# Kernel tuning notes

Hardware: AMD Instinct MI355X
Metric: run time of the kernel (lower is better)

The kernel has to match this reference:

```python
import jax, jax.numpy as jnp
import numpy as np

PATCH = 256
N = 50000
HC = 256  # height // PATCH
WC = 256  # width // PATCH

def _gauss_kernel():
    # GaussianSmoothing(channels=1, kernel_size=3, sigma=0.5)
    g = np.exp(-(((np.arange(3, dtype=np.float64) - 1.0) / 0.5) ** 2) / 2.0) / (0.5 * np.sqrt(2 * np.pi))
    k = np.outer(g, g)
    k = k / k.sum()
    return jnp.asarray(k, jnp.float32).reshape(1, 1, 3, 3)

def setup_inputs() -> dict:
    key = jax.random.key(0)
    ks = jax.random.split(key, 12)
    h = jax.random.normal(ks[0], (N, 1024), jnp.float32)
    # unique grid cells per patch (row-major), scaled back to pixel coords
    idx = jnp.arange(N, dtype=jnp.int64 if jax.config.jax_enable_x64 else jnp.int32)
    gx = idx % WC
    gy = idx // WC
    coords = jnp.stack([gx * PATCH, gy * PATCH], axis=1)
    eps = jax.random.normal(ks[1], (1, 1, HC, WC), jnp.float32)
    s = 0.02
    W1 = jax.random.normal(ks[2], (512, 1024), jnp.float32) * s
    b1 = jnp.zeros((512,), jnp.float32)
    W2a = jax.random.normal(ks[3], (256, 512), jnp.float32) * s
    b2a = jnp.zeros((256,), jnp.float32)
    W2b = jax.random.normal(ks[4], (256, 512), jnp.float32) * s
    b2b = jnp.zeros((256,), jnp.float32)
    W3 = jax.random.normal(ks[5], (2, 256), jnp.float32) * s
    b3 = jnp.zeros((2,), jnp.float32)
    Wc = jax.random.normal(ks[6], (2, 512), jnp.float32) * s
    bc = jnp.zeros((2,), jnp.float32)
    kernel = _gauss_kernel()
    return {"h": h, "coords": coords, "eps": eps,
            "W1": W1, "b1": b1, "W2a": W2a, "b2a": b2a, "W2b": W2b, "b2b": b2b,
            "W3": W3, "b3": b3, "Wc": Wc, "bc": bc, "kernel": kernel,
            "height": 65536, "width": 65536, "slide_label": 1}

def reference(h, coords, eps, W1, b1, W2a, b2a, W2b, b2b, W3, b3, Wc, bc, kernel, height, width, slide_label):
    hc, wc = height // PATCH, width // PATCH
    x = jax.nn.relu(h @ W1.T + b1)                      # [N,512] (dropout = eval identity)
    fa = jax.nn.sigmoid(x @ W2a.T + b2a)                # [N,256]
    fb = jnp.tanh(x @ W2b.T + b2b)                      # [N,256]
    params = (fa * fb) @ W3.T + b3                      # [N,2] -> (mu, logvar) per patch
    gx = coords[:, 0] // PATCH
    gy = coords[:, 1] // PATCH
    mu = jnp.zeros((1, hc, wc), x.dtype).at[0, gy, gx].set(params[:, 0])
    logvar = jnp.zeros((1, hc, wc), x.dtype).at[0, gy, gx].set(params[:, 1])
    prior_mu = jnp.array([-5.0, 0.0], x.dtype)[slide_label]
    prior_lv = jnp.array([-1.0, 3.0], x.dtype)[slide_label]
    kl_div = (prior_lv - logvar) / 2.0 + (logvar ** 2 + (prior_mu - mu) ** 2) / (2.0 * prior_lv ** 2) - 0.5
    mu_pad = jnp.pad(mu, ((0, 0), (1, 1), (1, 1)))[None]          # [1,1,hc+2,wc+2]
    mu_sm = jax.lax.conv_general_dilated(mu_pad, kernel, (1, 1), 'VALID')  # [1,1,hc,wc]
    samples = mu_sm + eps * jnp.exp(0.5 * logvar)                  # reparameterize, broadcast to [1,1,hc,wc]
    A = jax.nn.sigmoid(samples[0])                                 # [1,hc,wc]
    patch_A = A[0, gy, gx][None]                                   # gather -> [1,N]
    M = (patch_A @ x) / patch_A.sum()                              # [1,512]
    logits = M @ Wc.T + bc                                         # [1,n_classes]
    y_probs = jax.nn.softmax(logits, axis=1)
    top_idx = jax.lax.top_k(y_probs[:, 1], 1)[1]                   # top_k=1
    top_instance = logits[top_idx]                                 # [1,n_classes]
    Y_hat = jnp.argmax(top_instance, axis=1, keepdims=True)
    Y_prob = jax.nn.softmax(top_instance, axis=1)
    return (top_instance, Y_prob, Y_hat, kl_div, y_probs, patch_A)
```

## Files before the change

### kernel.cpp

```cpp
#include <hip/hip_runtime.h>
#include <hip/hip_bf16.h>
#include <cstdint>
#include <cstddef>

#define NPATCH 50000
#define GC 256

typedef __bf16 bf16x8 __attribute__((ext_vector_type(8)));
typedef float  f32x4  __attribute__((ext_vector_type(4)));
typedef float  f32x8  __attribute__((ext_vector_type(8)));

static constexpr size_t XB_OFF    = 0;
static constexpr size_t XB_BYTES  = (size_t)50048 * 512 * 2;
static constexpr size_t W1B_OFF   = XB_OFF + XB_BYTES;
static constexpr size_t W1B_BYTES = (size_t)512 * 1024 * 2;
static constexpr size_t W2AB_OFF  = W1B_OFF + W1B_BYTES;
static constexpr size_t W2X_BYTES = (size_t)256 * 512 * 2;
static constexpr size_t W2BB_OFF  = W2AB_OFF + W2X_BYTES;
static constexpr size_t MUG_OFF   = W2BB_OFF + W2X_BYTES;
static constexpr size_t LVG_OFF   = MUG_OFF + (size_t)65536 * 4;
static constexpr size_t AG_OFF    = LVG_OFF + (size_t)65536 * 4;
static constexpr size_t MPART_OFF = AG_OFF + (size_t)65536 * 4;
static constexpr size_t SUMA_OFF  = MPART_OFF + (size_t)512 * 4;
static constexpr size_t ZERO_BYTES = SUMA_OFF + 4 - MUG_OFF;

__device__ __forceinline__ unsigned short f2bf(float f) {
  union { float f; uint32_t u; } v; v.f = f;
  uint32_t u = v.u;
  uint32_t r = (u + 0x7FFFu + ((u >> 16) & 1u)) >> 16;
  return (unsigned short)r;
}
__device__ __forceinline__ float bf2f(uint32_t bits16) {
  union { uint32_t u; float f; } v; v.u = bits16 << 16; return v.f;
}
__device__ __forceinline__ unsigned short cvt_bf16(float f) {
  __bf16 b = (__bf16)f;
  return __builtin_bit_cast(unsigned short, b);
}
__device__ __forceinline__ void gld16(const void* g, void* l) {
  __builtin_amdgcn_global_load_lds(
      (const __attribute__((address_space(1))) void*)g,
      (__attribute__((address_space(3))) void*)l, 16, 0, 0);
}
__device__ __forceinline__ bf16x8 cvt8(const float4& f0, const float4& f1) {
  f32x8 fv;
  fv[0]=f0.x; fv[1]=f0.y; fv[2]=f0.z; fv[3]=f0.w;
  fv[4]=f1.x; fv[5]=f1.y; fv[6]=f1.z; fv[7]=f1.w;
  return __builtin_convertvector(fv, bf16x8);
}

__global__ void convert_weights(const float* __restrict__ W1,
                                const float* __restrict__ W2a,
                                const float* __restrict__ W2b,
                                unsigned short* __restrict__ W1b,
                                unsigned short* __restrict__ W2ab,
                                unsigned short* __restrict__ W2bb) {
  int i = blockIdx.x * 256 + threadIdx.x;
  if (i < 512 * 1024) W1b[i] = f2bf(W1[i]);
  if (i < 256 * 512) { W2ab[i] = f2bf(W2a[i]); W2bb[i] = f2bf(W2b[i]); }
}

__global__ __launch_bounds__(256) void gemm1(
    const float* __restrict__ h, const unsigned short* __restrict__ W1b,
    const float* __restrict__ b1, unsigned short* __restrict__ xb) {
  __shared__ __align__(16) unsigned short As[2][128 * 32];
  __shared__ __align__(16) unsigned short Bs[2][128 * 32];

  const int t  = threadIdx.x;
  const int l  = t & 63;
  const int w  = t >> 6;
  const int wr = w >> 1;
  const int wc = w & 1;
  const int g  = l >> 4;
  const int lr = l & 15;

  const int i = blockIdx.x;
  const int x = i & 7;
  const int s = i >> 3;
  const int n = s & 3;
  const int q = s >> 2;
  const int m = x + 8 * q;
  if (m >= 391) return;
  const int rowBase = m * 128;
  const int colBase = n * 128;

  const int ar = t >> 2;
  const int aj = t & 3;
  int gr0 = rowBase + ar;       if (gr0 >= NPATCH) gr0 = NPATCH - 1;
  int gr1 = rowBase + 64 + ar;  if (gr1 >= NPATCH) gr1 = NPATCH - 1;
  const float* asrc0 = h + (size_t)gr0 * 1024 + aj * 8;
  const float* asrc1 = h + (size_t)gr1 * 1024 + aj * 8;
  const unsigned short* bsrc0 = W1b + (size_t)(colBase + ar) * 1024 + aj * 8;
  const unsigned short* bsrc1 = bsrc0 + (size_t)64 * 1024;
  const int dst0 = t * 8;
  const int dst1 = 2048 + t * 8;

  f32x4 acc[4][4];
#pragma unroll
  for (int mm = 0; mm < 4; ++mm)
#pragma unroll
    for (int nn = 0; nn < 4; ++nn) acc[mm][nn] = (f32x4){0.f, 0.f, 0.f, 0.f};

  float4 s00, s01, s10, s11;
  {
    float4 t00 = *(const float4*)(asrc0 + 0);
    float4 t01 = *(const float4*)(asrc0 + 4);
    float4 t10 = *(const float4*)(asrc1 + 0);
    float4 t11 = *(const float4*)(asrc1 + 4);
    gld16(bsrc0, &Bs[0][dst0]);
    gld16(bsrc1, &Bs[0][dst1]);
    *(bf16x8*)&As[0][dst0] = cvt8(t00, t01);
    *(bf16x8*)&As[0][dst1] = cvt8(t10, t11);
    s00 = *(const float4*)(asrc0 + 32);
    s01 = *(const float4*)(asrc0 + 36);
    s10 = *(const float4*)(asrc1 + 32);
    s11 = *(const float4*)(asrc1 + 36);
  }
  __syncthreads();

  int cur = 0;
  for (int kt = 0; kt < 32; ++kt) {
    if (kt < 31) {
      gld16(bsrc0 + (kt + 1) * 32, &Bs[cur ^ 1][dst0]);
      gld16(bsrc1 + (kt + 1) * 32, &Bs[cur ^ 1][dst1]);
      *(bf16x8*)&As[cur ^ 1][dst0] = cvt8(s00, s01);
      *(bf16x8*)&As[cur ^ 1][dst1] = cvt8(s10, s11);
      if (kt < 30) {
        s00 = *(const float4*)(asrc0 + (kt + 2) * 32);
        s01 = *(const float4*)(asrc0 + (kt + 2) * 32 + 4);
        s10 = *(const float4*)(asrc1 + (kt + 2) * 32);
        s11 = *(const float4*)(asrc1 + (kt + 2) * 32 + 4);
      }
    }
    bf16x8 af[4], bfr[4];
#pragma unroll
    for (int mm = 0; mm < 4; ++mm)
      af[mm] = *(const bf16x8*)&As[cur][(wr * 64 + mm * 16 + lr) * 32 + g * 8];
#pragma unroll
    for (int nn = 0; nn < 4; ++nn)
      bfr[nn] = *(const bf16x8*)&Bs[cur][(wc * 64 + nn * 16 + lr) * 32 + g * 8];
#pragma unroll
    for (int mm = 0; mm < 4; ++mm)
#pragma unroll
      for (int nn = 0; nn < 4; ++nn)
        acc[mm][nn] = __builtin_amdgcn_mfma_f32_16x16x32_bf16(af[mm], bfr[nn], acc[mm][nn], 0, 0, 0);
    __syncthreads();
    cur ^= 1;
  }

  float b1v[4];
#pragma unroll
  for (int nn = 0; nn < 4; ++nn) b1v[nn] = b1[colBase + wc * 64 + nn * 16 + lr];
#pragma unroll
  for (int mm = 0; mm < 4; ++mm) {
    const int rb0 = rowBase + wr * 64 + mm * 16 + g * 4;
#pragma unroll
    for (int r = 0; r < 4; ++r) {
      const int row = rb0 + r;
      if (row < NPATCH) {
        unsigned short* xrow = xb + (size_t)row * 512 + colBase + wc * 64;
#pragma unroll
        for (int nn = 0; nn < 4; ++nn) {
          float v = acc[mm][nn][r] + b1v[nn];
          v = v > 0.f ? v : 0.f;
          xrow[nn * 16 + lr] = cvt_bf16(v);
        }
      }
    }
  }
}

__global__ __launch_bounds__(256, 2) void gemm2(
    const unsigned short* __restrict__ xb,
    const unsigned short* __restrict__ W2ab, const unsigned short* __restrict__ W2bb,
    const float* __restrict__ b2a, const float* __restrict__ b2b,
    const float* __restrict__ W3, const float* __restrict__ b3,
    const int* __restrict__ coords,
    float* __restrict__ mug, float* __restrict__ lvg) {
  __shared__ __align__(16) unsigned short xs[64 * 40];
  __shared__ __align__(16) unsigned short was[256 * 40];
  __shared__ __align__(16) unsigned short wbs[256 * 40];
  __shared__ float pmu_s[4][64];
  __shared__ float plv_s[4][64];

  const int t = threadIdx.x;
  const int l = t & 63;
  const int w = t >> 6;
  const int g = l >> 4, lr = l & 15;
  const int rowBase = blockIdx.x * 64;

  f32x4 aa[4][4], ab[4][4];
#pragma unroll
  for (int m = 0; m < 4; ++m)
#pragma unroll
    for (int n = 0; n < 4; ++n) {
      aa[m][n] = (f32x4){0.f, 0.f, 0.f, 0.f};
      ab[m][n] = (f32x4){0.f, 0.f, 0.f, 0.f};
    }

  const int xrow = t >> 2;
  const int xc0  = (t & 3) * 8;
  const int grow = rowBase + xrow;
  const bool xval = grow < NPATCH;

  for (int kt = 0; kt < 16; ++kt) {
    const int k0 = kt * 32;
    __syncthreads();
    if (xval) {
      *(int4*)&xs[xrow * 40 + xc0] = *(const int4*)(xb + (size_t)grow * 512 + k0 + xc0);
    } else {
      int4 z = {0, 0, 0, 0};
      *(int4*)&xs[xrow * 40 + xc0] = z;
    }
#pragma unroll
    for (int j = 0; j < 4; ++j) {
      int rrow = (t >> 2) + 64 * j;
      *(int4*)&was[rrow * 40 + xc0] = *(const int4*)(W2ab + (size_t)rrow * 512 + k0 + xc0);
      *(int4*)&wbs[rrow * 40 + xc0] = *(const int4*)(W2bb + (size_t)rrow * 512 + k0 + xc0);
    }
    __syncthreads();

    bf16x8 af[4], ba[4], bb[4];
#pragma unroll
    for (int m = 0; m < 4; ++m)
      af[m] = *(const bf16x8*)&xs[(m * 16 + lr) * 40 + g * 8];
#pragma unroll
    for (int n = 0; n < 4; ++n) {
      int brow = w * 64 + n * 16 + lr;
      ba[n] = *(const bf16x8*)&was[brow * 40 + g * 8];
      bb[n] = *(const bf16x8*)&wbs[brow * 40 + g * 8];
    }
#pragma unroll
    for (int m = 0; m < 4; ++m)
#pragma unroll
      for (int n = 0; n < 4; ++n) {
        aa[m][n] = __builtin_amdgcn_mfma_f32_16x16x32_bf16(af[m], ba[n], aa[m][n], 0, 0, 0);
        ab[m][n] = __builtin_amdgcn_mfma_f32_16x16x32_bf16(af[m], bb[n], ab[m][n], 0, 0, 0);
      }
  }

  float b2av[4], b2bv[4], w30v[4], w31v[4];
#pragma unroll
  for (int n = 0; n < 4; ++n) {
    int col = w * 64 + n * 16 + lr;
    b2av[n] = b2a[col]; b2bv[n] = b2b[col];
    w30v[n] = W3[col];  w31v[n] = W3[256 + col];
  }
#pragma unroll
  for (int m = 0; m < 4; ++m) {
#pragma unroll
    for (int r = 0; r < 4; ++r) {
      float pm = 0.f, pl = 0.f;
#pragma unroll
      for (int n = 0; n < 4; ++n) {
        float a = 1.f / (1.f + __expf(-(aa[m][n][r] + b2av[n])));
        float b = tanhf(ab[m][n][r] + b2bv[n]);
        float p = a * b;
        pm += p * w30v[n];
        pl += p * w31v[n];
      }
#pragma unroll
      for (int d = 1; d < 16; d <<= 1) {
        pm += __shfl_xor(pm, d, 64);
        pl += __shfl_xor(pl, d, 64);
      }
      if (lr == 0) {
        pmu_s[w][m * 16 + g * 4 + r] = pm;
        plv_s[w][m * 16 + g * 4 + r] = pl;
      }
    }
  }
  __syncthreads();
  if (t < 64) {
    float mu = pmu_s[0][t] + pmu_s[1][t] + pmu_s[2][t] + pmu_s[3][t] + b3[0];
    float lv = plv_s[0][t] + plv_s[1][t] + plv_s[2][t] + plv_s[3][t] + b3[1];
    int row = rowBase + t;
    if (row < NPATCH) {
      int gx = coords[2 * row] >> 8;
      int gy = coords[2 * row + 1] >> 8;
      int cell = gy * GC + gx;
      mug[cell] = mu;
      lvg[cell] = lv;
    }
  }
}

__global__ void grid_ops(const float* __restrict__ mug, const float* __restrict__ lvg,
                         const float* __restrict__ eps, const float* __restrict__ kern,
                         const int* __restrict__ slide, float* __restrict__ Ag,
                         float* __restrict__ out_kl) {
  int cell = blockIdx.x * 256 + threadIdx.x;
  int iy = cell >> 8, ix = cell & 255;
  float mu = mug[cell], lv = lvg[cell];
  int sl = slide[0];
  float pm  = (sl == 0) ? -5.0f : 0.0f;
  float plv = (sl == 0) ? -1.0f : 3.0f;
  float d = pm - mu;
  out_kl[cell] = (plv - lv) * 0.5f + (lv * lv + d * d) / (2.0f * plv * plv) - 0.5f;
  float s = 0.f;
#pragma unroll
  for (int dy = 0; dy < 3; ++dy) {
#pragma unroll
    for (int dx = 0; dx < 3; ++dx) {
      int y = iy + dy - 1, x = ix + dx - 1;
      if (y >= 0 && y < GC && x >= 0 && x < GC)
        s += mug[y * GC + x] * kern[dy * 3 + dx];
    }
  }
  float sample = s + eps[cell] * __expf(0.5f * lv);
  Ag[cell] = 1.f / (1.f + __expf(-sample));
}

__global__ __launch_bounds__(256) void patch_pass(
    const float* __restrict__ Ag, const int* __restrict__ coords,
    const unsigned short* __restrict__ xb, float* __restrict__ out_pA,
    float* __restrict__ Mpart, float* __restrict__ sumA) {
  __shared__ float als[256];
  __shared__ float swave[4];
  const int t = threadIdx.x;
  const int base = blockIdx.x * 256;
  const int row = base + t;
  float a = 0.f;
  if (row < NPATCH) {
    int gx = coords[2 * row] >> 8;
    int gy = coords[2 * row + 1] >> 8;
    a = Ag[gy * GC + gx];
    out_pA[row] = a;
  }
  als[t] = a;
  float sa = a;
#pragma unroll
  for (int d = 1; d < 64; d <<= 1) sa += __shfl_xor(sa, d, 64);
  if ((t & 63) == 0) swave[t >> 6] = sa;
  __syncthreads();
  if (t == 0) atomicAdd(sumA, swave[0] + swave[1] + swave[2] + swave[3]);

  const int nrows = min(256, NPATCH - base);
  float m0 = 0.f, m1 = 0.f;
  for (int r = 0; r < nrows; ++r) {
    float av = als[r];
    const uint32_t* p = (const uint32_t*)(xb + (size_t)(base + r) * 512);
    uint32_t v = p[t];
    m0 += av * bf2f(v & 0xFFFFu);
    m1 += av * bf2f(v >> 16);
  }
  atomicAdd(&Mpart[t * 2 + 0], m0);
  atomicAdd(&Mpart[t * 2 + 1], m1);
}

__global__ void finalize(const float* __restrict__ Mpart, const float* __restrict__ sumA,
                         const float* __restrict__ Wc, const float* __restrict__ bc,
                         float* __restrict__ out) {
  const int t = threadIdx.x;
  float s = sumA[0];
  float l0 = 0.f, l1 = 0.f;
#pragma unroll
  for (int j = 0; j < 8; ++j) {
    int c = t * 8 + j;
    float m = Mpart[c] / s;
    l0 += m * Wc[c];
    l1 += m * Wc[512 + c];
  }
#pragma unroll
  for (int d = 1; d < 64; d <<= 1) {
    l0 += __shfl_xor(l0, d, 64);
    l1 += __shfl_xor(l1, d, 64);
  }
  if (t == 0) {
    l0 += bc[0]; l1 += bc[1];
    float mx = fmaxf(l0, l1);
    float e0 = __expf(l0 - mx), e1 = __expf(l1 - mx);
    float inv = 1.f / (e0 + e1);
    float p0 = e0 * inv, p1 = e1 * inv;
    out[0] = l0; out[1] = l1;
    out[2] = p0; out[3] = p1;
    out[4] = (l1 > l0) ? 1.0f : 0.0f;
    out[65541] = p0; out[65542] = p1;
  }
}

extern "C" void kernel_launch(void* const* d_in, const int* in_sizes, int n_in,
                              void* d_out, int out_size, void* d_ws, size_t ws_size,
                              hipStream_t stream) {
  const float* h      = (const float*)d_in[0];
  const int*   coords = (const int*)d_in[1];
  const float* eps    = (const float*)d_in[2];
  const float* W1     = (const float*)d_in[3];
  const float* b1     = (const float*)d_in[4];
  const float* W2a    = (const float*)d_in[5];
  const float* b2a    = (const float*)d_in[6];
  const float* W2b    = (const float*)d_in[7];
  const float* b2b    = (const float*)d_in[8];
  const float* W3     = (const float*)d_in[9];
  const float* b3     = (const float*)d_in[10];
  const float* Wc     = (const float*)d_in[11];
  const float* bc     = (const float*)d_in[12];
  const float* kern   = (const float*)d_in[13];
  const int*   slide  = (const int*)d_in[16];
  float* out = (float*)d_out;
  char*  ws  = (char*)d_ws;

  unsigned short* xb   = (unsigned short*)(ws + XB_OFF);
  unsigned short* W1b  = (unsigned short*)(ws + W1B_OFF);
  unsigned short* W2ab = (unsigned short*)(ws + W2AB_OFF);
  unsigned short* W2bb = (unsigned short*)(ws + W2BB_OFF);
  float* mug   = (float*)(ws + MUG_OFF);
  float* lvg   = (float*)(ws + LVG_OFF);
  float* Ag    = (float*)(ws + AG_OFF);
  float* Mpart = (float*)(ws + MPART_OFF);
  float* sumA  = (float*)(ws + SUMA_OFF);

  hipMemsetAsync(ws + MUG_OFF, 0, ZERO_BYTES, stream);

  convert_weights<<<2048, 256, 0, stream>>>(W1, W2a, W2b, W1b, W2ab, W2bb);
  gemm1<<<1568, 256, 0, stream>>>(h, W1b, b1, xb);
  gemm2<<<782, 256, 0, stream>>>(xb, W2ab, W2bb, b2a, b2b, W3, b3, coords, mug, lvg);
  grid_ops<<<256, 256, 0, stream>>>(mug, lvg, eps, kern, slide, Ag, out + 5);
  patch_pass<<<196, 256, 0, stream>>>(Ag, coords, xb, out + 65543, Mpart, sumA);
  finalize<<<1, 64, 0, stream>>>(Mpart, sumA, Wc, bc, out);
}
```

Baseline: 212.1 us.

## Triple-buffer B tiles in gemm1 with one barrier per k-step

Rebuilds the gemm1 main loop around a three-stage shared-memory ring for the W1 tiles, with double-buffered activation tiles. Each k-step now has a single barrier guarded by a manual s_waitcnt vmcnt(6) instead of two __syncthreads, and the loop is fully unrolled. The goal is to keep global loads further ahead of the MFMA work and cut synchronisation stalls. The costs are more LDS per block, a hand-counted vmcnt that silently depends on the number of loads issued per step, and a few redundant clamped loads in the tail iterations.

Measured after the change: 218.7 us. 3.1% more time.

```diff
diff --git a/kernel.cpp b/kernel.cpp
--- a/kernel.cpp
+++ b/kernel.cpp
@@ -64,7 +64,7 @@
     const float* __restrict__ h, const unsigned short* __restrict__ W1b,
     const float* __restrict__ b1, unsigned short* __restrict__ xb) {
   __shared__ __align__(16) unsigned short As[2][128 * 32];
-  __shared__ __align__(16) unsigned short Bs[2][128 * 32];
+  __shared__ __align__(16) unsigned short Bs[3][128 * 32];
 
   const int t  = threadIdx.x;
   const int l  = t & 63;
@@ -103,12 +103,14 @@
 
   float4 s00, s01, s10, s11;
   {
+    gld16(bsrc0, &Bs[0][dst0]);
+    gld16(bsrc1, &Bs[0][dst1]);
+    gld16(bsrc0 + 32, &Bs[1][dst0]);
+    gld16(bsrc1 + 32, &Bs[1][dst1]);
     float4 t00 = *(const float4*)(asrc0 + 0);
     float4 t01 = *(const float4*)(asrc0 + 4);
     float4 t10 = *(const float4*)(asrc1 + 0);
     float4 t11 = *(const float4*)(asrc1 + 4);
-    gld16(bsrc0, &Bs[0][dst0]);
-    gld16(bsrc1, &Bs[0][dst1]);
     *(bf16x8*)&As[0][dst0] = cvt8(t00, t01);
     *(bf16x8*)&As[0][dst1] = cvt8(t10, t11);
     s00 = *(const float4*)(asrc0 + 32);
@@ -116,37 +118,34 @@
     s10 = *(const float4*)(asrc1 + 32);
     s11 = *(const float4*)(asrc1 + 36);
   }
-  __syncthreads();
-
-  int cur = 0;
+
+#pragma unroll
   for (int kt = 0; kt < 32; ++kt) {
-    if (kt < 31) {
-      gld16(bsrc0 + (kt + 1) * 32, &Bs[cur ^ 1][dst0]);
-      gld16(bsrc1 + (kt + 1) * 32, &Bs[cur ^ 1][dst1]);
-      *(bf16x8*)&As[cur ^ 1][dst0] = cvt8(s00, s01);
-      *(bf16x8*)&As[cur ^ 1][dst1] = cvt8(s10, s11);
-      if (kt < 30) {
-        s00 = *(const float4*)(asrc0 + (kt + 2) * 32);
-        s01 = *(const float4*)(asrc0 + (kt + 2) * 32 + 4);
-        s10 = *(const float4*)(asrc1 + (kt + 2) * 32);
-        s11 = *(const float4*)(asrc1 + (kt + 2) * 32 + 4);
-      }
-    }
+    asm volatile("s_waitcnt vmcnt(6) lgkmcnt(0)\n\ts_barrier" ::: "memory");
+    const int ksrc = (kt + 2 <= 31) ? (kt + 2) : 31;
+    gld16(bsrc0 + ksrc * 32, &Bs[(kt + 2) % 3][dst0]);
+    gld16(bsrc1 + ksrc * 32, &Bs[(kt + 2) % 3][dst1]);
+    *(bf16x8*)&As[(kt + 1) & 1][dst0] = cvt8(s00, s01);
+    *(bf16x8*)&As[(kt + 1) & 1][dst1] = cvt8(s10, s11);
+    s00 = *(const float4*)(asrc0 + ksrc * 32);
+    s01 = *(const float4*)(asrc0 + ksrc * 32 + 4);
+    s10 = *(const float4*)(asrc1 + ksrc * 32);
+    s11 = *(const float4*)(asrc1 + ksrc * 32 + 4);
     bf16x8 af[4], bfr[4];
 #pragma unroll
     for (int mm = 0; mm < 4; ++mm)
-      af[mm] = *(const bf16x8*)&As[cur][(wr * 64 + mm * 16 + lr) * 32 + g * 8];
+      af[mm] = *(const bf16x8*)&As[kt & 1][(wr * 64 + mm * 16 + lr) * 32 + g * 8];
 #pragma unroll
     for (int nn = 0; nn < 4; ++nn)
-      bfr[nn] = *(const bf16x8*)&Bs[cur][(wc * 64 + nn * 16 + lr) * 32 + g * 8];
+      bfr[nn] = *(const bf16x8*)&Bs[kt % 3][(wc * 64 + nn * 16 + lr) * 32 + g * 8];
 #pragma unroll
     for (int mm = 0; mm < 4; ++mm)
 #pragma unroll
       for (int nn = 0; nn < 4; ++nn)
         acc[mm][nn] = __builtin_amdgcn_mfma_f32_16x16x32_bf16(af[mm], bfr[nn], acc[mm][nn], 0, 0, 0);
-    __syncthreads();
-    cur ^= 1;
-  }
+  }
+  asm volatile("s_waitcnt vmcnt(0) lgkmcnt(0)" ::: "memory");
+  __syncthreads();
 
   float b1v[4];
 #pragma unroll
```

## Load GEMM1 operands directly into registers, dropping LDS staging

Applied to the files above, without the earlier changes.

gemm1 no longer stages the h and W1 tiles through shared memory. Each lane loads its MFMA fragments straight from global memory into registers, with one-step register double-buffering and no __syncthreads. The tile shrinks from 128x128 to 64x128, which doubles the grid and changes the block-to-tile mapping to spread work across XCDs. This removes LDS traffic and barriers, but gives up reuse of each loaded element across waves, so global/L2 traffic rises and the loads are strided 16-byte row accesses.

New measurement: 481.7 us. 2.27x slower.

```diff
diff --git a/kernel.cpp b/kernel.cpp
--- a/kernel.cpp
+++ b/kernel.cpp
@@ -37,11 +37,6 @@
   __bf16 b = (__bf16)f;
   return __builtin_bit_cast(unsigned short, b);
 }
-__device__ __forceinline__ void gld16(const void* g, void* l) {
-  __builtin_amdgcn_global_load_lds(
-      (const __attribute__((address_space(1))) void*)g,
-      (__attribute__((address_space(3))) void*)l, 16, 0, 0);
-}
 __device__ __forceinline__ bf16x8 cvt8(const float4& f0, const float4& f1) {
   f32x8 fv;
   fv[0]=f0.x; fv[1]=f0.y; fv[2]=f0.z; fv[3]=f0.w;
@@ -63,9 +58,6 @@
 __global__ __launch_bounds__(256) void gemm1(
     const float* __restrict__ h, const unsigned short* __restrict__ W1b,
     const float* __restrict__ b1, unsigned short* __restrict__ xb) {
-  __shared__ __align__(16) unsigned short As[2][128 * 32];
-  __shared__ __align__(16) unsigned short Bs[2][128 * 32];
-
   const int t  = threadIdx.x;
   const int l  = t & 63;
   const int w  = t >> 6;
@@ -74,86 +66,75 @@
   const int g  = l >> 4;
   const int lr = l & 15;
 
-  const int i = blockIdx.x;
-  const int x = i & 7;
-  const int s = i >> 3;
-  const int n = s & 3;
-  const int q = s >> 2;
-  const int m = x + 8 * q;
-  if (m >= 391) return;
-  const int rowBase = m * 128;
-  const int colBase = n * 128;
-
-  const int ar = t >> 2;
-  const int aj = t & 3;
-  int gr0 = rowBase + ar;       if (gr0 >= NPATCH) gr0 = NPATCH - 1;
-  int gr1 = rowBase + 64 + ar;  if (gr1 >= NPATCH) gr1 = NPATCH - 1;
-  const float* asrc0 = h + (size_t)gr0 * 1024 + aj * 8;
-  const float* asrc1 = h + (size_t)gr1 * 1024 + aj * 8;
-  const unsigned short* bsrc0 = W1b + (size_t)(colBase + ar) * 1024 + aj * 8;
-  const unsigned short* bsrc1 = bsrc0 + (size_t)64 * 1024;
-  const int dst0 = t * 8;
-  const int dst1 = 2048 + t * 8;
-
-  f32x4 acc[4][4];
-#pragma unroll
-  for (int mm = 0; mm < 4; ++mm)
+  const int i  = blockIdx.x;
+  const int x  = i & 7;
+  const int j  = i >> 3;
+  const int v  = x * 391 + j;
+  const int rt = v >> 2;
+  const int ct = v & 3;
+  const int rowBase = rt * 64;
+  const int colBase = ct * 128;
+
+  const float* ap[2];
+#pragma unroll
+  for (int mm = 0; mm < 2; ++mm) {
+    int r = rowBase + wr * 32 + mm * 16 + lr;
+    if (r >= NPATCH) r = NPATCH - 1;
+    ap[mm] = h + (size_t)r * 1024 + g * 8;
+  }
+  const unsigned short* bp[4];
+#pragma unroll
+  for (int nn = 0; nn < 4; ++nn) {
+    int c = colBase + wc * 64 + nn * 16 + lr;
+    bp[nn] = W1b + (size_t)c * 1024 + g * 8;
+  }
+
+  f32x4 acc[2][4];
+#pragma unroll
+  for (int mm = 0; mm < 2; ++mm)
 #pragma unroll
     for (int nn = 0; nn < 4; ++nn) acc[mm][nn] = (f32x4){0.f, 0.f, 0.f, 0.f};
 
-  float4 s00, s01, s10, s11;
-  {
-    float4 t00 = *(const float4*)(asrc0 + 0);
-    float4 t01 = *(const float4*)(asrc0 + 4);
-    float4 t10 = *(const float4*)(asrc1 + 0);
-    float4 t11 = *(const float4*)(asrc1 + 4);
-    gld16(bsrc0, &Bs[0][dst0]);
-    gld16(bsrc1, &Bs[0][dst1]);
-    *(bf16x8*)&As[0][dst0] = cvt8(t00, t01);
-    *(bf16x8*)&As[0][dst1] = cvt8(t10, t11);
-    s00 = *(const float4*)(asrc0 + 32);
-    s01 = *(const float4*)(asrc0 + 36);
-    s10 = *(const float4*)(asrc1 + 32);
-    s11 = *(const float4*)(asrc1 + 36);
-  }
-  __syncthreads();
-
-  int cur = 0;
+  float4 a0[2][2]; bf16x8 bq0[4];
+#pragma unroll
+  for (int mm = 0; mm < 2; ++mm) {
+    a0[mm][0] = *(const float4*)(ap[mm]);
+    a0[mm][1] = *(const float4*)(ap[mm] + 4);
+  }
+#pragma unroll
+  for (int nn = 0; nn < 4; ++nn) bq0[nn] = *(const bf16x8*)(bp[nn]);
+
+#pragma unroll 2
   for (int kt = 0; kt < 32; ++kt) {
-    if (kt < 31) {
-      gld16(bsrc0 + (kt + 1) * 32, &Bs[cur ^ 1][dst0]);
-      gld16(bsrc1 + (kt + 1) * 32, &Bs[cur ^ 1][dst1]);
-      *(bf16x8*)&As[cur ^ 1][dst0] = cvt8(s00, s01);
-      *(bf16x8*)&As[cur ^ 1][dst1] = cvt8(s10, s11);
-      if (kt < 30) {
-        s00 = *(const float4*)(asrc0 + (kt + 2) * 32);
-        s01 = *(const float4*)(asrc0 + (kt + 2) * 32 + 4);
-        s10 = *(const float4*)(asrc1 + (kt + 2) * 32);
-        s11 = *(const float4*)(asrc1 + (kt + 2) * 32 + 4);
-      }
-    }
-    bf16x8 af[4], bfr[4];
-#pragma unroll
-    for (int mm = 0; mm < 4; ++mm)
-      af[mm] = *(const bf16x8*)&As[cur][(wr * 64 + mm * 16 + lr) * 32 + g * 8];
-#pragma unroll
-    for (int nn = 0; nn < 4; ++nn)
-      bfr[nn] = *(const bf16x8*)&Bs[cur][(wc * 64 + nn * 16 + lr) * 32 + g * 8];
-#pragma unroll
-    for (int mm = 0; mm < 4; ++mm)
+    const int kn = (kt + 1 <= 31) ? (kt + 1) : 31;
+    float4 a1[2][2]; bf16x8 bq1[4];
+#pragma unroll
+    for (int mm = 0; mm < 2; ++mm) {
+      a1[mm][0] = *(const float4*)(ap[mm] + kn * 32);
+      a1[mm][1] = *(const float4*)(ap[mm] + kn * 32 + 4);
+    }
+#pragma unroll
+    for (int nn = 0; nn < 4; ++nn) bq1[nn] = *(const bf16x8*)(bp[nn] + kn * 32);
+    bf16x8 afr[2];
+#pragma unroll
+    for (int mm = 0; mm < 2; ++mm) afr[mm] = cvt8(a0[mm][0], a0[mm][1]);
+#pragma unroll
+    for (int mm = 0; mm < 2; ++mm)
 #pragma unroll
       for (int nn = 0; nn < 4; ++nn)
-        acc[mm][nn] = __builtin_amdgcn_mfma_f32_16x16x32_bf16(af[mm], bfr[nn], acc[mm][nn], 0, 0, 0);
-    __syncthreads();
-    cur ^= 1;
+        acc[mm][nn] = __builtin_amdgcn_mfma_f32_16x16x32_bf16(afr[mm], bq0[nn], acc[mm][nn], 0, 0, 0);
+#pragma unroll
+    for (int mm = 0; mm < 2; ++mm) { a0[mm][0] = a1[mm][0]; a0[mm][1] = a1[mm][1]; }
+#pragma unroll
+    for (int nn = 0; nn < 4; ++nn) bq0[nn] = bq1[nn];
   }
 
   float b1v[4];
 #pragma unroll
   for (int nn = 0; nn < 4; ++nn) b1v[nn] = b1[colBase + wc * 64 + nn * 16 + lr];
 #pragma unroll
-  for (int mm = 0; mm < 4; ++mm) {
-    const int rb0 = rowBase + wr * 64 + mm * 16 + g * 4;
+  for (int mm = 0; mm < 2; ++mm) {
+    const int rb0 = rowBase + wr * 32 + mm * 16 + g * 4;
 #pragma unroll
     for (int r = 0; r < 4; ++r) {
       const int row = rb0 + r;
@@ -161,9 +142,9 @@
         unsigned short* xrow = xb + (size_t)row * 512 + colBase + wc * 64;
 #pragma unroll
         for (int nn = 0; nn < 4; ++nn) {
-          float v = acc[mm][nn][r] + b1v[nn];
-          v = v > 0.f ? v : 0.f;
-          xrow[nn * 16 + lr] = cvt_bf16(v);
+          float vv = acc[mm][nn][r] + b1v[nn];
+          vv = vv > 0.f ? vv : 0.f;
+          xrow[nn * 16 + lr] = cvt_bf16(vv);
         }
       }
     }
@@ -413,7 +394,7 @@
   hipMemsetAsync(ws + MUG_OFF, 0, ZERO_BYTES, stream);
 
   convert_weights<<<2048, 256, 0, stream>>>(W1, W2a, W2b, W1b, W2ab, W2bb);
-  gemm1<<<1568, 256, 0, stream>>>(h, W1b, b1, xb);
+  gemm1<<<3128, 256, 0, stream>>>(h, W1b, b1, xb);
   gemm2<<<782, 256, 0, stream>>>(xb, W2ab, W2bb, b2a, b2b, W3, b3, coords, mug, lvg);
   grid_ops<<<256, 256, 0, stream>>>(mug, lvg, eps, kern, slide, Ag, out + 5);
   patch_pass<<<196, 256, 0, stream>>>(Ag, coords, xb, out + 65543, Mpart, sumA);
```

## Widen gemm1 tile to 128x256 so each fp32 h row is read twice

Applied to the files above, without the earlier changes.

gemm1 now computes 128x256 output tiles instead of 128x128, so each fp32 row of h is loaded and converted to bf16 by 2 blocks rather than 4. Each wave holds a 4x8 MFMA accumulator block, the B shared buffer doubles, and the grid drops to 782 blocks with a plain row/column mapping in place of the swizzled one. The aim is to cut the dominant global traffic from the large fp32 h matrix. The cost is much higher register use (128 accumulator floats), which launch_bounds(256,2) may force into spills, plus more LDS per block and fewer blocks to spread over the CUs.

Measured after the change: 202.9 us. 4.3% less time.

```diff
diff --git a/kernel.cpp b/kernel.cpp
--- a/kernel.cpp
+++ b/kernel.cpp
@@ -60,11 +60,11 @@
   if (i < 256 * 512) { W2ab[i] = f2bf(W2a[i]); W2bb[i] = f2bf(W2b[i]); }
 }
 
-__global__ __launch_bounds__(256) void gemm1(
+__global__ __launch_bounds__(256, 2) void gemm1(
     const float* __restrict__ h, const unsigned short* __restrict__ W1b,
     const float* __restrict__ b1, unsigned short* __restrict__ xb) {
   __shared__ __align__(16) unsigned short As[2][128 * 32];
-  __shared__ __align__(16) unsigned short Bs[2][128 * 32];
+  __shared__ __align__(16) unsigned short Bs[2][256 * 32];
 
   const int t  = threadIdx.x;
   const int l  = t & 63;
@@ -74,15 +74,10 @@
   const int g  = l >> 4;
   const int lr = l & 15;
 
-  const int i = blockIdx.x;
-  const int x = i & 7;
-  const int s = i >> 3;
-  const int n = s & 3;
-  const int q = s >> 2;
-  const int m = x + 8 * q;
-  if (m >= 391) return;
-  const int rowBase = m * 128;
-  const int colBase = n * 128;
+  const int rt = blockIdx.x >> 1;
+  const int ct = blockIdx.x & 1;
+  const int rowBase = rt * 128;
+  const int colBase = ct * 256;
 
   const int ar = t >> 2;
   const int aj = t & 3;
@@ -90,27 +85,30 @@
   int gr1 = rowBase + 64 + ar;  if (gr1 >= NPATCH) gr1 = NPATCH - 1;
   const float* asrc0 = h + (size_t)gr0 * 1024 + aj * 8;
   const float* asrc1 = h + (size_t)gr1 * 1024 + aj * 8;
-  const unsigned short* bsrc0 = W1b + (size_t)(colBase + ar) * 1024 + aj * 8;
-  const unsigned short* bsrc1 = bsrc0 + (size_t)64 * 1024;
-  const int dst0 = t * 8;
-  const int dst1 = 2048 + t * 8;
-
-  f32x4 acc[4][4];
+  const int adst0 = t * 8;
+  const int adst1 = 2048 + t * 8;
+
+  const unsigned short* bsrc[4];
+#pragma unroll
+  for (int r = 0; r < 4; ++r)
+    bsrc[r] = W1b + (size_t)(colBase + r * 64 + (t >> 2)) * 1024 + (t & 3) * 8;
+
+  f32x4 acc[4][8];
 #pragma unroll
   for (int mm = 0; mm < 4; ++mm)
 #pragma unroll
-    for (int nn = 0; nn < 4; ++nn) acc[mm][nn] = (f32x4){0.f, 0.f, 0.f, 0.f};
+    for (int nn = 0; nn < 8; ++nn) acc[mm][nn] = (f32x4){0.f, 0.f, 0.f, 0.f};
 
   float4 s00, s01, s10, s11;
   {
+#pragma unroll
+    for (int r = 0; r < 4; ++r) gld16(bsrc[r], &Bs[0][r * 2048 + t * 8]);
     float4 t00 = *(const float4*)(asrc0 + 0);
     float4 t01 = *(const float4*)(asrc0 + 4);
     float4 t10 = *(const float4*)(asrc1 + 0);
     float4 t11 = *(const float4*)(asrc1 + 4);
-    gld16(bsrc0, &Bs[0][dst0]);
-    gld16(bsrc1, &Bs[0][dst1]);
-    *(bf16x8*)&As[0][dst0] = cvt8(t00, t01);
-    *(bf16x8*)&As[0][dst1] = cvt8(t10, t11);
+    *(bf16x8*)&As[0][adst0] = cvt8(t00, t01);
+    *(bf16x8*)&As[0][adst1] = cvt8(t10, t11);
     s00 = *(const float4*)(asrc0 + 32);
     s01 = *(const float4*)(asrc0 + 36);
     s10 = *(const float4*)(asrc1 + 32);
@@ -121,10 +119,11 @@
   int cur = 0;
   for (int kt = 0; kt < 32; ++kt) {
     if (kt < 31) {
-      gld16(bsrc0 + (kt + 1) * 32, &Bs[cur ^ 1][dst0]);
-      gld16(bsrc1 + (kt + 1) * 32, &Bs[cur ^ 1][dst1]);
-      *(bf16x8*)&As[cur ^ 1][dst0] = cvt8(s00, s01);
-      *(bf16x8*)&As[cur ^ 1][dst1] = cvt8(s10, s11);
+#pragma unroll
+      for (int r = 0; r < 4; ++r)
+        gld16(bsrc[r] + (kt + 1) * 32, &Bs[cur ^ 1][r * 2048 + t * 8]);
+      *(bf16x8*)&As[cur ^ 1][adst0] = cvt8(s00, s01);
+      *(bf16x8*)&As[cur ^ 1][adst1] = cvt8(s10, s11);
       if (kt < 30) {
         s00 = *(const float4*)(asrc0 + (kt + 2) * 32);
         s01 = *(const float4*)(asrc0 + (kt + 2) * 32 + 4);
@@ -132,25 +131,25 @@
         s11 = *(const float4*)(asrc1 + (kt + 2) * 32 + 4);
       }
     }
-    bf16x8 af[4], bfr[4];
+    bf16x8 af[4], bfr[8];
 #pragma unroll
     for (int mm = 0; mm < 4; ++mm)
       af[mm] = *(const bf16x8*)&As[cur][(wr * 64 + mm * 16 + lr) * 32 + g * 8];
 #pragma unroll
-    for (int nn = 0; nn < 4; ++nn)
-      bfr[nn] = *(const bf16x8*)&Bs[cur][(wc * 64 + nn * 16 + lr) * 32 + g * 8];
+    for (int nn = 0; nn < 8; ++nn)
+      bfr[nn] = *(const bf16x8*)&Bs[cur][(wc * 128 + nn * 16 + lr) * 32 + g * 8];
 #pragma unroll
     for (int mm = 0; mm < 4; ++mm)
 #pragma unroll
-      for (int nn = 0; nn < 4; ++nn)
+      for (int nn = 0; nn < 8; ++nn)
         acc[mm][nn] = __builtin_amdgcn_mfma_f32_16x16x32_bf16(af[mm], bfr[nn], acc[mm][nn], 0, 0, 0);
     __syncthreads();
     cur ^= 1;
   }
 
-  float b1v[4];
-#pragma unroll
-  for (int nn = 0; nn < 4; ++nn) b1v[nn] = b1[colBase + wc * 64 + nn * 16 + lr];
+  float b1v[8];
+#pragma unroll
+  for (int nn = 0; nn < 8; ++nn) b1v[nn] = b1[colBase + wc * 128 + nn * 16 + lr];
 #pragma unroll
   for (int mm = 0; mm < 4; ++mm) {
     const int rb0 = rowBase + wr * 64 + mm * 16 + g * 4;
@@ -158,12 +157,12 @@
     for (int r = 0; r < 4; ++r) {
       const int row = rb0 + r;
       if (row < NPATCH) {
-        unsigned short* xrow = xb + (size_t)row * 512 + colBase + wc * 64;
-#pragma unroll
-        for (int nn = 0; nn < 4; ++nn) {
-          float v = acc[mm][nn][r] + b1v[nn];
-          v = v > 0.f ? v : 0.f;
-          xrow[nn * 16 + lr] = cvt_bf16(v);
+        unsigned short* xrow = xb + (size_t)row * 512 + colBase + wc * 128;
+#pragma unroll
+        for (int nn = 0; nn < 8; ++nn) {
+          float vv = acc[mm][nn][r] + b1v[nn];
+          vv = vv > 0.f ? vv : 0.f;
+          xrow[nn * 16 + lr] = cvt_bf16(vv);
         }
       }
     }
@@ -413,7 +412,7 @@
   hipMemsetAsync(ws + MUG_OFF, 0, ZERO_BYTES, stream);
 
   convert_weights<<<2048, 256, 0, stream>>>(W1, W2a, W2b, W1b, W2ab, W2bb);
-  gemm1<<<1568, 256, 0, stream>>>(h, W1b, b1, xb);
+  gemm1<<<782, 256, 0, stream>>>(h, W1b, b1, xb);
   gemm2<<<782, 256, 0, stream>>>(xb, W2ab, W2bb, b2a, b2b, W3, b3, coords, mug, lvg);
   grid_ops<<<256, 256, 0, stream>>>(mug, lvg, eps, kern, slide, Ag, out + 5);
   patch_pass<<<196, 256, 0, stream>>>(Ag, coords, xb, out + 65543, Mpart, sumA);
```
